# Kernel optimization log

Measured on AMD Instinct MI355X. Metric: run time of the kernel, lower is better.

Reference implementation:

```python
import jax, jax.numpy as jnp
import numpy as np

N_NODES = 100000
NODE_DIM = 64
IN_DIM_V = 128
N_LAYERS = 4
N_CLASSES = 40
N_EDGES = 1600000
LEAKY_SLOPE = 0.2
BN_EPS = 1e-5


def setup_inputs() -> dict:
    key = jax.random.key(0)
    ks = jax.random.split(key, 12)
    V = jax.random.normal(ks[0], (N_NODES, IN_DIM_V), dtype=jnp.float32)
    src = jax.random.randint(ks[1], (N_EDGES,), 0, N_NODES, dtype=jnp.int64 if jax.config.jax_enable_x64 else jnp.int32)
    dst = jax.random.randint(ks[2], (N_EDGES,), 0, N_NODES, dtype=jnp.int64 if jax.config.jax_enable_x64 else jnp.int32)
    s_in = 1.0 / np.sqrt(IN_DIM_V)
    s_h = 1.0 / np.sqrt(NODE_DIM)
    W_in = jax.random.normal(ks[3], (IN_DIM_V, NODE_DIM), dtype=jnp.float32) * s_in
    b_in = jnp.zeros((NODE_DIM,), jnp.float32)
    W_l = jax.random.normal(ks[4], (N_LAYERS, NODE_DIM, NODE_DIM), dtype=jnp.float32) * s_h
    b_l = jnp.zeros((N_LAYERS, NODE_DIM), jnp.float32)
    gamma = jnp.ones((N_LAYERS, NODE_DIM), jnp.float32)
    beta = jnp.zeros((N_LAYERS, NODE_DIM), jnp.float32)
    W_out = jax.random.normal(ks[5], (NODE_DIM, N_CLASSES), dtype=jnp.float32) * s_h
    b_out = jnp.zeros((N_CLASSES,), jnp.float32)
    return {"V": V, "src": src, "dst": dst, "W_in": W_in, "b_in": b_in,
            "W_l": W_l, "b_l": b_l, "gamma": gamma, "beta": beta,
            "W_out": W_out, "b_out": b_out}


def _batchnorm(x, g, b):
    # BatchNorm1d in training mode: biased variance over the node axis
    m = jnp.mean(x, axis=0)
    v = jnp.mean(jnp.square(x - m), axis=0)
    return (x - m) * jax.lax.rsqrt(v + BN_EPS) * g + b


def reference(V, src, dst, W_in, b_in, W_l, b_l, gamma, beta, W_out, b_out):
    N = V.shape[0]
    ones = jnp.ones((src.shape[0],), V.dtype)
    deg_out = jax.ops.segment_sum(ones, src, num_segments=N)
    deg_in = jax.ops.segment_sum(ones, dst, num_segments=N)
    norm_src = jax.lax.rsqrt(jnp.clip(deg_out, 1.0))[:, None]  # [N,1]
    norm_dst = jax.lax.rsqrt(jnp.clip(deg_in, 1.0))[:, None]

    # trans_input: linear embedding in_dim_V -> node_dim
    h = V @ W_in + b_in  # [N, node_dim]

    for l in range(N_LAYERS):
        h_in = h
        # dropout p=0 / eval mode -> identity
        # GraphConv norm='both': D^{-1/2} A D^{-1/2} X W + b
        m = h * norm_src                                      # [N, d]
        agg = jax.ops.segment_sum(m[src], dst, num_segments=N)  # gather-scatter over edges
        agg = agg * norm_dst
        hc = agg @ W_l[l] + b_l[l]
        hc = _batchnorm(hc, gamma[l], beta[l])
        hc = jnp.where(hc >= 0, hc, LEAKY_SLOPE * hc)
        h = hc + h_in  # residual (cell index hard-wired to 1 in source)

    logits = h @ W_out + b_out  # trans_output: node_dim -> n_classes
    return jax.nn.log_softmax(logits, axis=1)
```

## Files before the change

### kernel.cpp

```cpp
#include <hip/hip_runtime.h>
#include <math.h>


#define LEAKY_SLOPE 0.2f
#define BN_EPS 1e-5f
#define DEG_CAP 48


__global__ __launch_bounds__(256, 8)
void hist_kernel(const int* __restrict__ src, int* __restrict__ cnt_src, int E) {
  int i = blockIdx.x * blockDim.x + threadIdx.x;
  int stride = gridDim.x * blockDim.x;
  for (; i < E; i += stride) {
    atomicAdd(&cnt_src[src[i]], 1);
  }
}

__global__ __launch_bounds__(256, 8)
void fill_kernel(const int* __restrict__ src, const int* __restrict__ dst,
                 int* __restrict__ cnt_dst, int* __restrict__ bucket, int E, int N) {
  int gid = blockIdx.x * blockDim.x + threadIdx.x;
  int stride = gridDim.x * blockDim.x;
  int chunk = (N + 15) >> 4;
  for (int pass = 0; pass < 16; ++pass) {
    int lo = pass * chunk;
    int hi = lo + chunk;
    for (int i = gid; i < E; i += stride) {
      int d = dst[i];
      if (d >= lo && d < hi) {
        int pos = atomicAdd(&cnt_dst[d], 1);
        if (pos < DEG_CAP) bucket[d * DEG_CAP + pos] = src[i];
      }
    }
  }
}

__global__ __launch_bounds__(256, 8)
void norms_kernel(const int* __restrict__ cnt_src, const int* __restrict__ cnt_dst,
                  float* __restrict__ norm_src, float* __restrict__ norm_dst, int N) {
  int i = blockIdx.x * blockDim.x + threadIdx.x;
  if (i < N) {
    norm_src[i] = rsqrtf(fmaxf((float)cnt_src[i], 1.0f));
    norm_dst[i] = rsqrtf(fmaxf((float)cnt_dst[i], 1.0f));
  }
}

__global__ __launch_bounds__(256) __attribute__((amdgpu_waves_per_eu(3, 4)))
void input_gemm_kernel(const float* __restrict__ V, const float* __restrict__ W_in,
                       const float* __restrict__ b_in, const float* __restrict__ norm_src,
                       float* __restrict__ h, float* __restrict__ hs, int N) {
  __shared__ __align__(16) float sW[128][64];
  __shared__ __align__(16) float sA[32][132];
  int tid = threadIdx.x;
  int c0 = (tid & 15) * 4;
  int rp = tid >> 4;
  int base = blockIdx.x * 32;

  float4 b4 = *(const float4*)&b_in[c0];

  #pragma unroll
  for (int it = 0; it < 8; it++) {
    int i = tid + it * 256;
    int r = i >> 4, cc = (i & 15) * 4;
    *(float4*)&sW[r][cc] = *(const float4*)&W_in[r * 64 + cc];
  }
  #pragma unroll
  for (int it = 0; it < 4; it++) {
    int i = tid + it * 256;
    int r = i >> 5, cc = (i & 31) * 4;
    int n = base + r;
    float4 v = make_float4(0.f, 0.f, 0.f, 0.f);
    if (n < N) v = *(const float4*)&V[(size_t)n * 128 + cc];
    *(float4*)&sA[r][cc] = v;
  }
  __syncthreads();

  int r0 = rp * 2, r1 = rp * 2 + 1;
  float acc0[4] = {0.f, 0.f, 0.f, 0.f};
  float acc1[4] = {0.f, 0.f, 0.f, 0.f};
  #pragma unroll 4
  for (int d0 = 0; d0 < 128; d0 += 4) {
    float4 wr0 = *(const float4*)&sW[d0 + 0][c0];
    float4 wr1 = *(const float4*)&sW[d0 + 1][c0];
    float4 wr2 = *(const float4*)&sW[d0 + 2][c0];
    float4 wr3 = *(const float4*)&sW[d0 + 3][c0];
    float4 a0 = *(const float4*)&sA[r0][d0];
    float4 a1 = *(const float4*)&sA[r1][d0];
    acc0[0] += a0.x * wr0.x + a0.y * wr1.x + a0.z * wr2.x + a0.w * wr3.x;
    acc0[1] += a0.x * wr0.y + a0.y * wr1.y + a0.z * wr2.y + a0.w * wr3.y;
    acc0[2] += a0.x * wr0.z + a0.y * wr1.z + a0.z * wr2.z + a0.w * wr3.z;
    acc0[3] += a0.x * wr0.w + a0.y * wr1.w + a0.z * wr2.w + a0.w * wr3.w;
    acc1[0] += a1.x * wr0.x + a1.y * wr1.x + a1.z * wr2.x + a1.w * wr3.x;
    acc1[1] += a1.x * wr0.y + a1.y * wr1.y + a1.z * wr2.y + a1.w * wr3.y;
    acc1[2] += a1.x * wr0.z + a1.y * wr1.z + a1.z * wr2.z + a1.w * wr3.z;
    acc1[3] += a1.x * wr0.w + a1.y * wr1.w + a1.z * wr2.w + a1.w * wr3.w;
  }

  int n0 = base + r0, n1 = base + r1;
  if (n0 < N) {
    float4 o = make_float4(acc0[0] + b4.x, acc0[1] + b4.y, acc0[2] + b4.z, acc0[3] + b4.w);
    *(float4*)&h[(size_t)n0 * 64 + c0] = o;
    float ns = norm_src[n0];
    float4 s = make_float4(o.x * ns, o.y * ns, o.z * ns, o.w * ns);
    *(float4*)&hs[(size_t)n0 * 64 + c0] = s;
  }
  if (n1 < N) {
    float4 o = make_float4(acc1[0] + b4.x, acc1[1] + b4.y, acc1[2] + b4.z, acc1[3] + b4.w);
    *(float4*)&h[(size_t)n1 * 64 + c0] = o;
    float ns = norm_src[n1];
    float4 s = make_float4(o.x * ns, o.y * ns, o.z * ns, o.w * ns);
    *(float4*)&hs[(size_t)n1 * 64 + c0] = s;
  }
}

__global__ __launch_bounds__(256, 8)
void agg_kernel(const float* __restrict__ hs, const float* __restrict__ norm_dst,
                const int* __restrict__ cnt_dst, const int* __restrict__ bucket,
                float* __restrict__ agg, int N) {
  int wid = __builtin_amdgcn_readfirstlane(blockIdx.x * 4 + (threadIdx.x >> 6));
  int lane = threadIdx.x & 63;
  if (wid >= N) return;
  int len = cnt_dst[wid];
  float nd = norm_dst[wid];
  const int* bkt = bucket + wid * DEG_CAP;
  float a0=0.f,a1=0.f,a2=0.f,a3=0.f,a4=0.f,a5=0.f,a6=0.f,a7=0.f;
  for (int j = 0; j < len; j += 8) {
    int s0=0,s1=0,s2=0,s3=0,s4=0,s5=0,s6=0,s7=0;
    if (j + 0 < len) s0 = bkt[j + 0];
    if (j + 1 < len) s1 = bkt[j + 1];
    if (j + 2 < len) s2 = bkt[j + 2];
    if (j + 3 < len) s3 = bkt[j + 3];
    if (j + 4 < len) s4 = bkt[j + 4];
    if (j + 5 < len) s5 = bkt[j + 5];
    if (j + 6 < len) s6 = bkt[j + 6];
    if (j + 7 < len) s7 = bkt[j + 7];
    if (j + 0 < len) a0 += hs[(size_t)s0 * 64 + lane];
    if (j + 1 < len) a1 += hs[(size_t)s1 * 64 + lane];
    if (j + 2 < len) a2 += hs[(size_t)s2 * 64 + lane];
    if (j + 3 < len) a3 += hs[(size_t)s3 * 64 + lane];
    if (j + 4 < len) a4 += hs[(size_t)s4 * 64 + lane];
    if (j + 5 < len) a5 += hs[(size_t)s5 * 64 + lane];
    if (j + 6 < len) a6 += hs[(size_t)s6 * 64 + lane];
    if (j + 7 < len) a7 += hs[(size_t)s7 * 64 + lane];
  }
  float acc = ((a0 + a1) + (a2 + a3)) + ((a4 + a5) + (a6 + a7));
  agg[(size_t)wid * 64 + lane] = acc * nd;
}

__global__ __launch_bounds__(256) __attribute__((amdgpu_waves_per_eu(4, 4)))
void gemm_stats_kernel(const float* __restrict__ agg, const float* __restrict__ W,
                       const float* __restrict__ b, float* __restrict__ hc,
                       float* __restrict__ stats, int N) {
  __shared__ __align__(16) float sW[64][64];
  __shared__ __align__(16) float sA[64][68];
  int tid = threadIdx.x;
  int lane = tid & 63;
  int wv = tid >> 6;
  int cg = lane & 15;
  int ng = lane >> 4;
  int nrow0 = wv * 16 + ng * 4;
  int base = blockIdx.x * 64;

  #pragma unroll
  for (int it = 0; it < 4; it++) {
    int i = tid + it * 256;
    int r = i >> 4, c4 = (i & 15) * 4;
    *(float4*)&sW[r][c4] = *(const float4*)&W[r * 64 + c4];
  }
  #pragma unroll
  for (int it = 0; it < 4; it++) {
    int i = tid + it * 256;
    int r = i >> 4, c4 = (i & 15) * 4;
    int n = base + r;
    float4 v = make_float4(0.f, 0.f, 0.f, 0.f);
    if (n < N) v = *(const float4*)&agg[(size_t)n * 64 + c4];
    *(float4*)&sA[r][c4] = v;
  }
  __syncthreads();

  float4 b4 = *(const float4*)&b[cg * 4];

  float acc[4][4];
  #pragma unroll
  for (int i = 0; i < 4; i++)
    #pragma unroll
    for (int c = 0; c < 4; c++) acc[i][c] = 0.f;

  #pragma unroll 4
  for (int d0 = 0; d0 < 64; d0 += 4) {
    float4 wr0 = *(const float4*)&sW[d0 + 0][cg * 4];
    float4 wr1 = *(const float4*)&sW[d0 + 1][cg * 4];
    float4 wr2 = *(const float4*)&sW[d0 + 2][cg * 4];
    float4 wr3 = *(const float4*)&sW[d0 + 3][cg * 4];
    #pragma unroll
    for (int i = 0; i < 4; i++) {
      float4 av = *(const float4*)&sA[nrow0 + i][d0];
      acc[i][0] += av.x * wr0.x + av.y * wr1.x + av.z * wr2.x + av.w * wr3.x;
      acc[i][1] += av.x * wr0.y + av.y * wr1.y + av.z * wr2.y + av.w * wr3.y;
      acc[i][2] += av.x * wr0.z + av.y * wr1.z + av.z * wr2.z + av.w * wr3.z;
      acc[i][3] += av.x * wr0.w + av.y * wr1.w + av.z * wr2.w + av.w * wr3.w;
    }
  }

  float st_s0=0.f,st_s1=0.f,st_s2=0.f,st_s3=0.f;
  float st_q0=0.f,st_q1=0.f,st_q2=0.f,st_q3=0.f;
  #pragma unroll
  for (int i = 0; i < 4; i++) {
    int n = base + nrow0 + i;
    if (n < N) {
      float4 o;
      o.x = acc[i][0] + b4.x; o.y = acc[i][1] + b4.y;
      o.z = acc[i][2] + b4.z; o.w = acc[i][3] + b4.w;
      *(float4*)&hc[(size_t)n * 64 + cg * 4] = o;
      st_s0 += o.x; st_s1 += o.y; st_s2 += o.z; st_s3 += o.w;
      st_q0 += o.x * o.x; st_q1 += o.y * o.y;
      st_q2 += o.z * o.z; st_q3 += o.w * o.w;
    }
  }

  __syncthreads();
  int rr = wv * 4 + ng;
  *(float4*)&sA[rr][cg * 4]      = make_float4(st_s0, st_s1, st_s2, st_s3);
  *(float4*)&sA[16 + rr][cg * 4] = make_float4(st_q0, st_q1, st_q2, st_q3);
  __syncthreads();
  if (tid < 64) {
    float s = 0.f, q = 0.f;
    #pragma unroll
    for (int r = 0; r < 16; r++) { s += sA[r][tid]; q += sA[16 + r][tid]; }
    atomicAdd(&stats[tid], s);
    atomicAdd(&stats[64 + tid], q);
  }
}

__global__ __launch_bounds__(256, 8)
void apply_kernel(const float* __restrict__ hc, const float* __restrict__ stats,
                  const float* __restrict__ gamma, const float* __restrict__ beta,
                  const float* __restrict__ norm_src, float* __restrict__ h,
                  float* __restrict__ hs, int N, int write_hs) {
  __shared__ float s_scale[64];
  __shared__ float s_shift[64];
  int tid = threadIdx.x;
  if (tid < 64) {
    float s = stats[tid];
    float ss = stats[64 + tid];
    float invN = 1.0f / (float)N;
    float mean = s * invN;
    float var = fmaxf(ss * invN - mean * mean, 0.0f);
    float scale = gamma[tid] * rsqrtf(var + BN_EPS);
    s_scale[tid] = scale;
    s_shift[tid] = beta[tid] - mean * scale;
  }
  __syncthreads();
  int total4 = N * 16;
  int i = blockIdx.x * blockDim.x + threadIdx.x;
  int stride = gridDim.x * blockDim.x;
  for (; i < total4; i += stride) {
    float4 v = ((const float4*)hc)[i];
    float4 r = ((const float4*)h)[i];
    int cb = (i * 4) & 63;
    int n = i >> 4;
    float o0 = v.x * s_scale[cb + 0] + s_shift[cb + 0];
    float o1 = v.y * s_scale[cb + 1] + s_shift[cb + 1];
    float o2 = v.z * s_scale[cb + 2] + s_shift[cb + 2];
    float o3 = v.w * s_scale[cb + 3] + s_shift[cb + 3];
    o0 = (o0 >= 0.f) ? o0 : LEAKY_SLOPE * o0;
    o1 = (o1 >= 0.f) ? o1 : LEAKY_SLOPE * o1;
    o2 = (o2 >= 0.f) ? o2 : LEAKY_SLOPE * o2;
    o3 = (o3 >= 0.f) ? o3 : LEAKY_SLOPE * o3;
    float4 oh;
    oh.x = o0 + r.x; oh.y = o1 + r.y; oh.z = o2 + r.z; oh.w = o3 + r.w;
    ((float4*)h)[i] = oh;
    if (write_hs) {
      float nsc = norm_src[n];
      float4 os;
      os.x = oh.x * nsc; os.y = oh.y * nsc; os.z = oh.z * nsc; os.w = oh.w * nsc;
      ((float4*)hs)[i] = os;
    }
  }
}

__global__ __launch_bounds__(256, 4)
void out_kernel(const float* __restrict__ h, const float* __restrict__ W_out,
                const float* __restrict__ b_out, float* __restrict__ out, int N) {
  __shared__ float sWoT[40][65];
  int tid = threadIdx.x;
  for (int i = tid; i < 2560; i += 256) {
    int d = i / 40;
    int c = i - d * 40;
    sWoT[c][d] = W_out[i];
  }
  __syncthreads();
  int gw = (int)((blockIdx.x * blockDim.x + tid) >> 6);
  int nw = (int)((gridDim.x * blockDim.x) >> 6);
  int lane = tid & 63;
  int cc = (lane < 40) ? lane : 39;
  float bias = (lane < 40) ? b_out[lane] : 0.f;
  const float* wrow = &sWoT[cc][0];
  for (int n = gw; n < N; n += nw) {
    int nsg = __builtin_amdgcn_readfirstlane(n);
    const float* hrow = h + (size_t)nsg * 64;
    float acc = bias;
    #pragma unroll
    for (int d = 0; d < 64; d++) acc += hrow[d] * wrow[d];
    float lg = (lane < 40) ? acc : -INFINITY;
    float m = lg;
    #pragma unroll
    for (int off = 32; off; off >>= 1) m = fmaxf(m, __shfl_xor(m, off));
    float e = (lane < 40) ? expf(acc - m) : 0.f;
    float s = e;
    #pragma unroll
    for (int off = 32; off; off >>= 1) s += __shfl_xor(s, off);
    float lse = m + logf(s);
    if (lane < 40) out[(size_t)nsg * 40 + lane] = acc - lse;
  }
}

extern "C" void kernel_launch(void* const* d_in, const int* in_sizes, int n_in,
                              void* d_out, int out_size, void* d_ws, size_t ws_size,
                              hipStream_t stream) {
  const float* V     = (const float*)d_in[0];
  const int*   src   = (const int*)d_in[1];
  const int*   dst   = (const int*)d_in[2];
  const float* W_in  = (const float*)d_in[3];
  const float* b_in  = (const float*)d_in[4];
  const float* W_l   = (const float*)d_in[5];
  const float* b_l   = (const float*)d_in[6];
  const float* gamma = (const float*)d_in[7];
  const float* beta  = (const float*)d_in[8];
  const float* W_out = (const float*)d_in[9];
  const float* b_out = (const float*)d_in[10];
  float* out = (float*)d_out;

  const int N = in_sizes[0] / 128;
  const int E = in_sizes[1];
  const int NL = 4;

  char* p = (char*)d_ws;
  auto alloc = [&](size_t bytes) {
    void* r = (void*)p;
    p += (bytes + 255) & ~(size_t)255;
    return r;
  };
  float* h       = (float*)alloc((size_t)N * 64 * 4);
  float* agg     = (float*)alloc((size_t)N * 64 * 4);
  float* hc      = (float*)alloc((size_t)N * 64 * 4);
  int*   bucket  = (int*)alloc((size_t)N * DEG_CAP * 4);
  int*   cnt_src = (int*)alloc((size_t)N * 4);
  int*   cnt_dst = (int*)alloc((size_t)N * 4);
  float* nrm_src = (float*)alloc((size_t)N * 4);
  float* nrm_dst = (float*)alloc((size_t)N * 4);
  float* stats   = (float*)alloc(128 * 4);
  (void)ws_size;
  float* hs = hc;

  hipMemsetAsync(cnt_src, 0, (size_t)N * 4, stream);
  hipMemsetAsync(cnt_dst, 0, (size_t)N * 4, stream);

  hist_kernel<<<2048, 256, 0, stream>>>(src, cnt_src, E);
  fill_kernel<<<2048, 256, 0, stream>>>(src, dst, cnt_dst, bucket, E, N);
  norms_kernel<<<(N + 255) / 256, 256, 0, stream>>>(cnt_src, cnt_dst, nrm_src, nrm_dst, N);

  input_gemm_kernel<<<(N + 31) / 32, 256, 0, stream>>>(V, W_in, b_in, nrm_src, h, hs, N);

  for (int l = 0; l < NL; l++) {
    agg_kernel<<<(N + 3) / 4, 256, 0, stream>>>(hs, nrm_dst, cnt_dst, bucket, agg, N);
    hipMemsetAsync(stats, 0, 128 * 4, stream);
    gemm_stats_kernel<<<(N + 63) / 64, 256, 0, stream>>>(agg, W_l + (size_t)l * 64 * 64,
                                                         b_l + (size_t)l * 64, hc, stats, N);
    apply_kernel<<<2048, 256, 0, stream>>>(hc, stats, gamma + (size_t)l * 64,
                                           beta + (size_t)l * 64, nrm_src, h, hs, N,
                                           (l < NL - 1) ? 1 : 0);
  }

  out_kernel<<<1024, 256, 0, stream>>>(h, W_out, b_out, out, N);
}
```

Measured before the change: 973.1 us.

## Store gathered features as bf16 and partition histogram/fill by XCD-aligned node ranges

The scaled node features that the aggregation kernel gathers are now stored in bf16, which halves the bytes fetched per edge in the gather-heavy aggregation. The bf16 buffer gets its own workspace slot instead of aliasing hc. The histogram and bucket-fill kernels now have each group of blocks (block id mod 8) handle only one eighth of the node range. This replaces the 16 sequential passes in fill with a single pass and is meant to keep atomics local to a cache partition. In exchange, features lose precision, and each edge index is read eight times.

```diff
diff --git a/kernel.cpp b/kernel.cpp
--- a/kernel.cpp
+++ b/kernel.cpp
@@ -6,31 +6,45 @@
 #define BN_EPS 1e-5f
 #define DEG_CAP 48
 
-
-__global__ __launch_bounds__(256, 8)
-void hist_kernel(const int* __restrict__ src, int* __restrict__ cnt_src, int E) {
-  int i = blockIdx.x * blockDim.x + threadIdx.x;
-  int stride = gridDim.x * blockDim.x;
+__device__ __forceinline__ unsigned short f2bf(float f) {
+  unsigned int x = __float_as_uint(f);
+  unsigned int r = (x + 0x7FFFu + ((x >> 16) & 1u)) >> 16;
+  return (unsigned short)r;
+}
+__device__ __forceinline__ float bf2f(unsigned short u) {
+  return __uint_as_float((unsigned int)u << 16);
+}
+
+__global__ __launch_bounds__(256, 8)
+void hist_kernel(const int* __restrict__ src, int* __restrict__ cnt_src, int E, int N) {
+  int bid = blockIdx.x;
+  int w = bid & 7;
+  int chunk = (N + 7) >> 3;
+  int lo = w * chunk;
+  int hi = min(lo + chunk, N);
+  int i = (bid >> 3) * blockDim.x + threadIdx.x;
+  int stride = (gridDim.x >> 3) * blockDim.x;
   for (; i < E; i += stride) {
-    atomicAdd(&cnt_src[src[i]], 1);
+    int s = src[i];
+    if (s >= lo && s < hi) atomicAdd(&cnt_src[s], 1);
   }
 }
 
 __global__ __launch_bounds__(256, 8)
 void fill_kernel(const int* __restrict__ src, const int* __restrict__ dst,
                  int* __restrict__ cnt_dst, int* __restrict__ bucket, int E, int N) {
-  int gid = blockIdx.x * blockDim.x + threadIdx.x;
-  int stride = gridDim.x * blockDim.x;
-  int chunk = (N + 15) >> 4;
-  for (int pass = 0; pass < 16; ++pass) {
-    int lo = pass * chunk;
-    int hi = lo + chunk;
-    for (int i = gid; i < E; i += stride) {
-      int d = dst[i];
-      if (d >= lo && d < hi) {
-        int pos = atomicAdd(&cnt_dst[d], 1);
-        if (pos < DEG_CAP) bucket[d * DEG_CAP + pos] = src[i];
-      }
+  int bid = blockIdx.x;
+  int w = bid & 7;
+  int chunk = (N + 7) >> 3;
+  int lo = w * chunk;
+  int hi = min(lo + chunk, N);
+  int i = (bid >> 3) * blockDim.x + threadIdx.x;
+  int stride = (gridDim.x >> 3) * blockDim.x;
+  for (; i < E; i += stride) {
+    int d = dst[i];
+    if (d >= lo && d < hi) {
+      int pos = atomicAdd(&cnt_dst[d], 1);
+      if (pos < DEG_CAP) bucket[d * DEG_CAP + pos] = src[i];
     }
   }
 }
@@ -48,7 +62,7 @@
 __global__ __launch_bounds__(256) __attribute__((amdgpu_waves_per_eu(3, 4)))
 void input_gemm_kernel(const float* __restrict__ V, const float* __restrict__ W_in,
                        const float* __restrict__ b_in, const float* __restrict__ norm_src,
-                       float* __restrict__ h, float* __restrict__ hs, int N) {
+                       float* __restrict__ h, unsigned short* __restrict__ hs, int N) {
   __shared__ __align__(16) float sW[128][64];
   __shared__ __align__(16) float sA[32][132];
   int tid = threadIdx.x;
@@ -101,20 +115,20 @@
     float4 o = make_float4(acc0[0] + b4.x, acc0[1] + b4.y, acc0[2] + b4.z, acc0[3] + b4.w);
     *(float4*)&h[(size_t)n0 * 64 + c0] = o;
     float ns = norm_src[n0];
-    float4 s = make_float4(o.x * ns, o.y * ns, o.z * ns, o.w * ns);
-    *(float4*)&hs[(size_t)n0 * 64 + c0] = s;
+    ushort4 s = make_ushort4(f2bf(o.x * ns), f2bf(o.y * ns), f2bf(o.z * ns), f2bf(o.w * ns));
+    *(ushort4*)&hs[(size_t)n0 * 64 + c0] = s;
   }
   if (n1 < N) {
     float4 o = make_float4(acc1[0] + b4.x, acc1[1] + b4.y, acc1[2] + b4.z, acc1[3] + b4.w);
     *(float4*)&h[(size_t)n1 * 64 + c0] = o;
     float ns = norm_src[n1];
-    float4 s = make_float4(o.x * ns, o.y * ns, o.z * ns, o.w * ns);
-    *(float4*)&hs[(size_t)n1 * 64 + c0] = s;
-  }
-}
-
-__global__ __launch_bounds__(256, 8)
-void agg_kernel(const float* __restrict__ hs, const float* __restrict__ norm_dst,
+    ushort4 s = make_ushort4(f2bf(o.x * ns), f2bf(o.y * ns), f2bf(o.z * ns), f2bf(o.w * ns));
+    *(ushort4*)&hs[(size_t)n1 * 64 + c0] = s;
+  }
+}
+
+__global__ __launch_bounds__(256, 8)
+void agg_kernel(const unsigned short* __restrict__ hs, const float* __restrict__ norm_dst,
                 const int* __restrict__ cnt_dst, const int* __restrict__ bucket,
                 float* __restrict__ agg, int N) {
   int wid = __builtin_amdgcn_readfirstlane(blockIdx.x * 4 + (threadIdx.x >> 6));
@@ -134,14 +148,23 @@
     if (j + 5 < len) s5 = bkt[j + 5];
     if (j + 6 < len) s6 = bkt[j + 6];
     if (j + 7 < len) s7 = bkt[j + 7];
-    if (j + 0 < len) a0 += hs[(size_t)s0 * 64 + lane];
-    if (j + 1 < len) a1 += hs[(size_t)s1 * 64 + lane];
-    if (j + 2 < len) a2 += hs[(size_t)s2 * 64 + lane];
-    if (j + 3 < len) a3 += hs[(size_t)s3 * 64 + lane];
-    if (j + 4 < len) a4 += hs[(size_t)s4 * 64 + lane];
-    if (j + 5 < len) a5 += hs[(size_t)s5 * 64 + lane];
-    if (j + 6 < len) a6 += hs[(size_t)s6 * 64 + lane];
-    if (j + 7 < len) a7 += hs[(size_t)s7 * 64 + lane];
+    unsigned short h0=0,h1=0,h2=0,h3=0,h4=0,h5=0,h6=0,h7=0;
+    if (j + 0 < len) h0 = hs[(size_t)s0 * 64 + lane];
+    if (j + 1 < len) h1 = hs[(size_t)s1 * 64 + lane];
+    if (j + 2 < len) h2 = hs[(size_t)s2 * 64 + lane];
+    if (j + 3 < len) h3 = hs[(size_t)s3 * 64 + lane];
+    if (j + 4 < len) h4 = hs[(size_t)s4 * 64 + lane];
+    if (j + 5 < len) h5 = hs[(size_t)s5 * 64 + lane];
+    if (j + 6 < len) h6 = hs[(size_t)s6 * 64 + lane];
+    if (j + 7 < len) h7 = hs[(size_t)s7 * 64 + lane];
+    if (j + 0 < len) a0 += bf2f(h0);
+    if (j + 1 < len) a1 += bf2f(h1);
+    if (j + 2 < len) a2 += bf2f(h2);
+    if (j + 3 < len) a3 += bf2f(h3);
+    if (j + 4 < len) a4 += bf2f(h4);
+    if (j + 5 < len) a5 += bf2f(h5);
+    if (j + 6 < len) a6 += bf2f(h6);
+    if (j + 7 < len) a7 += bf2f(h7);
   }
   float acc = ((a0 + a1) + (a2 + a3)) + ((a4 + a5) + (a6 + a7));
   agg[(size_t)wid * 64 + lane] = acc * nd;
@@ -236,7 +259,7 @@
 void apply_kernel(const float* __restrict__ hc, const float* __restrict__ stats,
                   const float* __restrict__ gamma, const float* __restrict__ beta,
                   const float* __restrict__ norm_src, float* __restrict__ h,
-                  float* __restrict__ hs, int N, int write_hs) {
+                  unsigned short* __restrict__ hs, int N, int write_hs) {
   __shared__ float s_scale[64];
   __shared__ float s_shift[64];
   int tid = threadIdx.x;
@@ -272,9 +295,9 @@
     ((float4*)h)[i] = oh;
     if (write_hs) {
       float nsc = norm_src[n];
-      float4 os;
-      os.x = oh.x * nsc; os.y = oh.y * nsc; os.z = oh.z * nsc; os.w = oh.w * nsc;
-      ((float4*)hs)[i] = os;
+      ushort4 os = make_ushort4(f2bf(oh.x * nsc), f2bf(oh.y * nsc),
+                                f2bf(oh.z * nsc), f2bf(oh.w * nsc));
+      ((ushort4*)hs)[i] = os;
     }
   }
 }
@@ -341,22 +364,22 @@
     p += (bytes + 255) & ~(size_t)255;
     return r;
   };
-  float* h       = (float*)alloc((size_t)N * 64 * 4);
-  float* agg     = (float*)alloc((size_t)N * 64 * 4);
-  float* hc      = (float*)alloc((size_t)N * 64 * 4);
-  int*   bucket  = (int*)alloc((size_t)N * DEG_CAP * 4);
-  int*   cnt_src = (int*)alloc((size_t)N * 4);
-  int*   cnt_dst = (int*)alloc((size_t)N * 4);
-  float* nrm_src = (float*)alloc((size_t)N * 4);
-  float* nrm_dst = (float*)alloc((size_t)N * 4);
-  float* stats   = (float*)alloc(128 * 4);
+  float*          h       = (float*)alloc((size_t)N * 64 * 4);
+  float*          agg     = (float*)alloc((size_t)N * 64 * 4);
+  float*          hc      = (float*)alloc((size_t)N * 64 * 4);
+  unsigned short* hs      = (unsigned short*)alloc((size_t)N * 64 * 2);
+  int*            bucket  = (int*)alloc((size_t)N * DEG_CAP * 4);
+  int*            cnt_src = (int*)alloc((size_t)N * 4);
+  int*            cnt_dst = (int*)alloc((size_t)N * 4);
+  float*          nrm_src = (float*)alloc((size_t)N * 4);
+  float*          nrm_dst = (float*)alloc((size_t)N * 4);
+  float*          stats   = (float*)alloc(128 * 4);
   (void)ws_size;
-  float* hs = hc;
 
   hipMemsetAsync(cnt_src, 0, (size_t)N * 4, stream);
   hipMemsetAsync(cnt_dst, 0, (size_t)N * 4, stream);
 
-  hist_kernel<<<2048, 256, 0, stream>>>(src, cnt_src, E);
+  hist_kernel<<<2048, 256, 0, stream>>>(src, cnt_src, E, N);
   fill_kernel<<<2048, 256, 0, stream>>>(src, dst, cnt_dst, bucket, E, N);
   norms_kernel<<<(N + 255) / 256, 256, 0, stream>>>(cnt_src, cnt_dst, nrm_src, nrm_dst, N);
 
```

Result: faster. 923.7 us (-5.1%).
